# Kernel tuning notes

Hardware: AMD Instinct MI355X
Metric: run time of the kernel (lower is better)

## Reference

```python
import jax, jax.numpy as jnp
import numpy as np

TEMPERATURE = 0.07
B, D = 8192, 256

def _l2norm(x, axis=-1, eps=1e-12):
    # matches torch F.normalize(p=2): x / max(||x||, eps)
    n = jnp.sqrt(jnp.sum(x * x, axis=axis, keepdims=True))
    return x / jnp.maximum(n, eps)

def setup_inputs() -> dict:
    key = jax.random.key(0)
    k1, k2, k3 = jax.random.split(key, 3)
    return {
        "h_emb": jax.random.normal(k1, (B, D), dtype=jnp.float32),
        "r_emb": jax.random.normal(k2, (B, D), dtype=jnp.float32),
        "t_emb": jax.random.normal(k3, (B, D), dtype=jnp.float32),
    }

def reference(h_emb, r_emb, t_emb):
    # query = normalize(h + r); positives/negatives = normalize(t)
    q = _l2norm(h_emb + r_emb, axis=1)          # [B, D]
    t = _l2norm(t_emb, axis=1)                  # [B, D]
    # Dense in-batch similarity. The original builds logits = [pos, off-diag negs];
    # since the diagonal of sim IS the positive similarity, cross-entropy with
    # label 0 equals logsumexp over the full row minus the diagonal entry.
    sim = jnp.einsum('bd,nd->bn', q, t) / TEMPERATURE   # [B, B]
    pos = jnp.diagonal(sim)                              # [B]
    loss = jnp.mean(jax.nn.logsumexp(sim, axis=1) - pos)
    return loss
```

## Files before the change

### kernel.cpp

```cpp
#include <hip/hip_runtime.h>
#include <hip/hip_bf16.h>

#define B_DIM 8192
#define D_DIM 256
#define GRID_GEMM 512
#define NT 16

constexpr float INV_T = 14.285714285714286f;

typedef __bf16 bf16x8 __attribute__((ext_vector_type(8)));
typedef float  f32x4  __attribute__((ext_vector_type(4)));

#define GLOBAL_U32(p) ((const __attribute__((address_space(1))) unsigned int*)(p))
#define LDS_U32(p)    ((__attribute__((address_space(3))) unsigned int*)(p))

#define WAITCNT_VM0 0x0F70

__device__ inline unsigned short f2bf(float f) {
    union { float f; unsigned u; } x; x.f = f;
    unsigned r = x.u + 0x7fffu + ((x.u >> 16) & 1u);
    return (unsigned short)(r >> 16);
}

__global__ __launch_bounds__(256) void norm_kernel(
    const float* __restrict__ h, const float* __restrict__ r,
    const float* __restrict__ t,
    unsigned short* __restrict__ qws, unsigned short* __restrict__ tws,
    float* __restrict__ rowsum, float* __restrict__ diagsum, int* __restrict__ ticket)
{
    if (blockIdx.x == 0) {
        float4* rs4 = (float4*)rowsum;
#pragma unroll
        for (int i = 0; i < 8; ++i)
            rs4[threadIdx.x * 8 + i] = make_float4(0.f, 0.f, 0.f, 0.f);
        if (threadIdx.x == 0) { *diagsum = 0.f; *ticket = 0; }
    }

    const int wave = threadIdx.x >> 6;
    const int lane = threadIdx.x & 63;
    const int wg   = blockIdx.x * 4 + wave;

    const int kst  = lane >> 3;
    const int krun = (lane >> 1) & 3;
    const int sub8 = lane & 1;

#pragma unroll
    for (int i = 0; i < 2; ++i) {
        const int row = wg * 2 + i;
        {
            float4 a = ((const float4*)h)[row * 64 + lane];
            float4 b = ((const float4*)r)[row * 64 + lane];
            float4 v = make_float4(a.x + b.x, a.y + b.y, a.z + b.z, a.w + b.w);
            float s = v.x * v.x + v.y * v.y + v.z * v.z + v.w * v.w;
#pragma unroll
            for (int off = 32; off; off >>= 1) s += __shfl_xor(s, off, 64);
            float scale = INV_T / fmaxf(sqrtf(s), 1e-12f);
            ushort4 o;
            o.x = f2bf(v.x * scale); o.y = f2bf(v.y * scale);
            o.z = f2bf(v.z * scale); o.w = f2bf(v.w * scale);
            size_t slot16 = ((size_t)((row >> 4) * 8 + kst) * 64
                             + (size_t)(krun * 16 + (row & 15)));
            *(ushort4*)((unsigned char*)qws + slot16 * 16 + sub8 * 8) = o;
        }
        {
            float4 v = ((const float4*)t)[row * 64 + lane];
            float s = v.x * v.x + v.y * v.y + v.z * v.z + v.w * v.w;
#pragma unroll
            for (int off = 32; off; off >>= 1) s += __shfl_xor(s, off, 64);
            float scale = 1.0f / fmaxf(sqrtf(s), 1e-12f);
            ushort4 o;
            o.x = f2bf(v.x * scale); o.y = f2bf(v.y * scale);
            o.z = f2bf(v.z * scale); o.w = f2bf(v.w * scale);
            size_t slot16 = ((size_t)((row >> 4) * 8 + kst) * 64
                             + (size_t)(krun * 16 + (row & 15)));
            *(ushort4*)((unsigned char*)tws + slot16 * 16 + sub8 * 8) = o;
        }
    }
}

__global__ __launch_bounds__(256, 2) void gemm_lse_kernel(
    const unsigned char* __restrict__ qws, const unsigned char* __restrict__ tws,
    float* __restrict__ rowsum, float* __restrict__ diagsum,
    int* __restrict__ ticket, float* __restrict__ out)
{
    __shared__ __align__(16) unsigned char ldsB[4][32 * 512];
    __shared__ float wred[4];
    __shared__ int lastflag;

    const int tid  = threadIdx.x;
    const int lane = tid & 63;
    const int w    = tid >> 6;
    const int l15  = lane & 15;
    const int hi4  = lane >> 4;

    const int cc   = blockIdx.x & 15;
    const int rb   = blockIdx.x >> 4;
    const int row0 = rb * 256 + w * 64;
    const int col0 = cc * 512;
    const int tile0 = cc * 16;

#define STAGE(st, bufi)                                                      \
    {                                                                        \
        const unsigned char* gs = tws + (size_t)(tile0 + (st)) * 16384;      \
        _Pragma("unroll")                                                    \
        for (int it = 0; it < 4; ++it)                                       \
            __builtin_amdgcn_global_load_lds(                                \
                GLOBAL_U32(gs + (it * 256 + tid) * 16),                      \
                LDS_U32(&ldsB[bufi][(it * 256 + tid) * 16]), 16, 0, 0);      \
    }

    STAGE(0, 0);
    STAGE(1, 1);

    bf16x8 a[4][8];
    {
        const unsigned char* abase = qws + (size_t)row0 * 512 + lane * 16;
#pragma unroll
        for (int r = 0; r < 4; ++r)
#pragma unroll
            for (int kst = 0; kst < 8; ++kst)
                a[r][kst] = *(const bf16x8*)(abase + r * 8192 + kst * 1024);
    }

    float rowacc[16] = {};
    float diagacc = 0.f;

#define PROCESS_TILE(t)                                                      \
    {                                                                        \
        const unsigned char* bbuf = ldsB[(t) & 3] + lane * 16;               \
        f32x4 acc[4][2] = {};                                                \
        _Pragma("unroll")                                                    \
        for (int kst = 0; kst < 8; ++kst) {                                  \
            bf16x8 b0 = *(const bf16x8*)(bbuf + kst * 1024);                 \
            bf16x8 b1 = *(const bf16x8*)(bbuf + 8192 + kst * 1024);          \
            _Pragma("unroll")                                                \
            for (int r = 0; r < 4; ++r) {                                    \
                acc[r][0] = __builtin_amdgcn_mfma_f32_16x16x32_bf16(         \
                                a[r][kst], b0, acc[r][0], 0, 0, 0);          \
                acc[r][1] = __builtin_amdgcn_mfma_f32_16x16x32_bf16(         \
                                a[r][kst], b1, acc[r][1], 0, 0, 0);          \
            }                                                                \
        }                                                                    \
        _Pragma("unroll")                                                    \
        for (int r = 0; r < 4; ++r)                                          \
            _Pragma("unroll")                                                \
            for (int g = 0; g < 4; ++g)                                      \
                rowacc[r * 4 + g] += __expf(acc[r][0][g] - INV_T)            \
                                   + __expf(acc[r][1][g] - INV_T);           \
        const int c0t = col0 + (t) * 32;                                     \
        if (c0t == row0) {                                                   \
            _Pragma("unroll")                                                \
            for (int g = 0; g < 4; ++g)                                      \
                if (l15 == hi4 * 4 + g)                                      \
                    diagacc += acc[0][0][g] + acc[1][1][g];                  \
        }                                                                    \
        if (c0t == row0 + 32) {                                              \
            _Pragma("unroll")                                                \
            for (int g = 0; g < 4; ++g)                                      \
                if (l15 == hi4 * 4 + g)                                      \
                    diagacc += acc[2][0][g] + acc[3][1][g];                  \
        }                                                                    \
    }

    for (int r = 0; r < 8; ++r) {
        __builtin_amdgcn_s_waitcnt(WAITCNT_VM0);
        __builtin_amdgcn_s_barrier();
        if (r < 7) {
            STAGE(2 * r + 2, (2 * r + 2) & 3);
            STAGE(2 * r + 3, (2 * r + 3) & 3);
        }
        PROCESS_TILE(2 * r);
        PROCESS_TILE(2 * r + 1);
    }

#pragma unroll
    for (int rr = 0; rr < 16; ++rr) {
        float s = rowacc[rr];
        s += __shfl_xor(s, 1, 64);
        s += __shfl_xor(s, 2, 64);
        s += __shfl_xor(s, 4, 64);
        s += __shfl_xor(s, 8, 64);
        if (l15 == 0) {
            int grow = row0 + (rr >> 2) * 16 + hi4 * 4 + (rr & 3);
            atomicAdd(&rowsum[grow], s);
        }
    }

    float dsum = diagacc;
#pragma unroll
    for (int off = 32; off; off >>= 1) dsum += __shfl_xor(dsum, off, 64);
    if (lane == 0 && dsum != 0.f) atomicAdd(diagsum, dsum);

    __syncthreads();
    if (tid == 0) {
        __threadfence();
        int old = __hip_atomic_fetch_add(ticket, 1, __ATOMIC_ACQ_REL,
                                         __HIP_MEMORY_SCOPE_AGENT);
        lastflag = (old == GRID_GEMM - 1);
    }
    __syncthreads();
    if (!lastflag) return;

    float lsum = 0.f;
    for (int rr = tid; rr < B_DIM; rr += 256) {
        float rs = __hip_atomic_load(&rowsum[rr], __ATOMIC_RELAXED,
                                     __HIP_MEMORY_SCOPE_AGENT);
        lsum += __logf(rs);
    }
#pragma unroll
    for (int off = 32; off; off >>= 1) lsum += __shfl_xor(lsum, off, 64);
    if (lane == 0) wred[w] = lsum;
    __syncthreads();
    if (tid == 0) {
        float ds = __hip_atomic_load(diagsum, __ATOMIC_RELAXED,
                                     __HIP_MEMORY_SCOPE_AGENT);
        float total = wred[0] + wred[1] + wred[2] + wred[3]
                    + (float)B_DIM * INV_T
                    - ds;
        out[0] = total / (float)B_DIM;
    }
}

extern "C" void kernel_launch(void* const* d_in, const int* in_sizes, int n_in,
                              void* d_out, int out_size, void* d_ws, size_t ws_size,
                              hipStream_t stream)
{
    const float* h = (const float*)d_in[0];
    const float* r = (const float*)d_in[1];
    const float* t = (const float*)d_in[2];

    unsigned char* ws = (unsigned char*)d_ws;
    unsigned short* qws = (unsigned short*)ws;
    unsigned short* tws = (unsigned short*)(ws + 4u * 1024 * 1024);
    float* rowsum  = (float*)(ws + 8u * 1024 * 1024);
    float* diagsum = (float*)(ws + 8u * 1024 * 1024 + 32u * 1024);
    int*   ticket  = (int*)  (ws + 8u * 1024 * 1024 + 32u * 1024 + 16);

    norm_kernel<<<1024, 256, 0, stream>>>(h, r, t, qws, tws, rowsum, diagsum, ticket);
    gemm_lse_kernel<<<GRID_GEMM, 256, 0, stream>>>(
        (const unsigned char*)qws, (const unsigned char*)tws,
        rowsum, diagsum, ticket, (float*)d_out);
}
```

Baseline: 125.5 us.

## Give each wave private double-buffered B staging to remove block barriers

Replaces the block-wide shared 4-stage B buffer and per-round s_barrier with per-wave private double buffers. Each wave loads its own copy of every 16-column group via global_load_lds and waits with a partial vmcnt instead of synchronising the whole block. This removes barrier stalls between waves, but each wave now fetches the full B tile itself, so global/L2 traffic for B is four times higher. Correctness also relies on the wave-local ordering of the LDS DMA against ds reads.

Result: slower. 131.8 us (+5.0%).

```diff
diff --git a/kernel.cpp b/kernel.cpp
--- a/kernel.cpp
+++ b/kernel.cpp
@@ -5,6 +5,7 @@
 #define D_DIM 256
 #define GRID_GEMM 512
 #define NT 16
+#define NGRP 32
 
 constexpr float INV_T = 14.285714285714286f;
 
@@ -14,7 +15,7 @@
 #define GLOBAL_U32(p) ((const __attribute__((address_space(1))) unsigned int*)(p))
 #define LDS_U32(p)    ((__attribute__((address_space(3))) unsigned int*)(p))
 
-#define WAITCNT_VM0 0x0F70
+#define WAITCNT_VM8 0x0F78
 
 __device__ inline unsigned short f2bf(float f) {
     union { float f; unsigned u; } x; x.f = f;
@@ -83,7 +84,7 @@
     float* __restrict__ rowsum, float* __restrict__ diagsum,
     int* __restrict__ ticket, float* __restrict__ out)
 {
-    __shared__ __align__(16) unsigned char ldsB[4][32 * 512];
+    __shared__ __align__(16) unsigned char ldsB[4][2][8192];
     __shared__ float wred[4];
     __shared__ int lastflag;
 
@@ -97,20 +98,18 @@
     const int rb   = blockIdx.x >> 4;
     const int row0 = rb * 256 + w * 64;
     const int col0 = cc * 512;
-    const int tile0 = cc * 16;
-
-#define STAGE(st, bufi)                                                      \
+
+#define STAGE_W(g, bufi)                                                     \
     {                                                                        \
-        const unsigned char* gs = tws + (size_t)(tile0 + (st)) * 16384;      \
+        const unsigned char* gs = tws + ((size_t)cc * 32 + (g)) * 8192;      \
         _Pragma("unroll")                                                    \
-        for (int it = 0; it < 4; ++it)                                       \
+        for (int it = 0; it < 8; ++it)                                       \
             __builtin_amdgcn_global_load_lds(                                \
-                GLOBAL_U32(gs + (it * 256 + tid) * 16),                      \
-                LDS_U32(&ldsB[bufi][(it * 256 + tid) * 16]), 16, 0, 0);      \
-    }
-
-    STAGE(0, 0);
-    STAGE(1, 1);
+                GLOBAL_U32(gs + (it * 64 + lane) * 16),                      \
+                LDS_U32(&ldsB[w][bufi][(it * 64 + lane) * 16]), 16, 0, 0);   \
+    }
+
+    STAGE_W(0, 0);
 
     bf16x8 a[4][8];
     {
@@ -125,52 +124,47 @@
     float rowacc[16] = {};
     float diagacc = 0.f;
 
-#define PROCESS_TILE(t)                                                      \
-    {                                                                        \
-        const unsigned char* bbuf = ldsB[(t) & 3] + lane * 16;               \
-        f32x4 acc[4][2] = {};                                                \
-        _Pragma("unroll")                                                    \
-        for (int kst = 0; kst < 8; ++kst) {                                  \
-            bf16x8 b0 = *(const bf16x8*)(bbuf + kst * 1024);                 \
-            bf16x8 b1 = *(const bf16x8*)(bbuf + 8192 + kst * 1024);          \
-            _Pragma("unroll")                                                \
-            for (int r = 0; r < 4; ++r) {                                    \
-                acc[r][0] = __builtin_amdgcn_mfma_f32_16x16x32_bf16(         \
-                                a[r][kst], b0, acc[r][0], 0, 0, 0);          \
-                acc[r][1] = __builtin_amdgcn_mfma_f32_16x16x32_bf16(         \
-                                a[r][kst], b1, acc[r][1], 0, 0, 0);          \
-            }                                                                \
-        }                                                                    \
-        _Pragma("unroll")                                                    \
-        for (int r = 0; r < 4; ++r)                                          \
-            _Pragma("unroll")                                                \
-            for (int g = 0; g < 4; ++g)                                      \
-                rowacc[r * 4 + g] += __expf(acc[r][0][g] - INV_T)            \
-                                   + __expf(acc[r][1][g] - INV_T);           \
-        const int c0t = col0 + (t) * 32;                                     \
-        if (c0t == row0) {                                                   \
-            _Pragma("unroll")                                                \
-            for (int g = 0; g < 4; ++g)                                      \
-                if (l15 == hi4 * 4 + g)                                      \
-                    diagacc += acc[0][0][g] + acc[1][1][g];                  \
-        }                                                                    \
-        if (c0t == row0 + 32) {                                              \
-            _Pragma("unroll")                                                \
-            for (int g = 0; g < 4; ++g)                                      \
-                if (l15 == hi4 * 4 + g)                                      \
-                    diagacc += acc[2][0][g] + acc[3][1][g];                  \
-        }                                                                    \
-    }
-
-    for (int r = 0; r < 8; ++r) {
-        __builtin_amdgcn_s_waitcnt(WAITCNT_VM0);
-        __builtin_amdgcn_s_barrier();
-        if (r < 7) {
-            STAGE(2 * r + 2, (2 * r + 2) & 3);
-            STAGE(2 * r + 3, (2 * r + 3) & 3);
-        }
-        PROCESS_TILE(2 * r);
-        PROCESS_TILE(2 * r + 1);
+    for (int t = 0; t < NT; ++t) {
+        f32x4 acc[4][2] = {};
+#pragma unroll
+        for (int cg = 0; cg < 2; ++cg) {
+            const int g = t * 2 + cg;
+            const int gn = (g + 1 < NGRP) ? g + 1 : NGRP - 1;
+            STAGE_W(gn, (g + 1) & 1);
+            __builtin_amdgcn_s_waitcnt(WAITCNT_VM8);
+            __builtin_amdgcn_sched_barrier(0);
+
+            const unsigned char* bbuf = &ldsB[w][g & 1][0] + lane * 16;
+#pragma unroll
+            for (int kst = 0; kst < 8; ++kst) {
+                bf16x8 b = *(const bf16x8*)(bbuf + kst * 1024);
+#pragma unroll
+                for (int r = 0; r < 4; ++r)
+                    acc[r][cg] = __builtin_amdgcn_mfma_f32_16x16x32_bf16(
+                                     a[r][kst], b, acc[r][cg], 0, 0, 0);
+            }
+        }
+
+#pragma unroll
+        for (int r = 0; r < 4; ++r)
+#pragma unroll
+            for (int g2 = 0; g2 < 4; ++g2)
+                rowacc[r * 4 + g2] += __expf(acc[r][0][g2] - INV_T)
+                                    + __expf(acc[r][1][g2] - INV_T);
+
+        const int c0t = col0 + t * 32;
+        if (c0t == row0) {
+#pragma unroll
+            for (int g2 = 0; g2 < 4; ++g2)
+                if (l15 == hi4 * 4 + g2)
+                    diagacc += acc[0][0][g2] + acc[1][1][g2];
+        }
+        if (c0t == row0 + 32) {
+#pragma unroll
+            for (int g2 = 0; g2 < 4; ++g2)
+                if (l15 == hi4 * 4 + g2)
+                    diagacc += acc[2][0][g2] + acc[3][1][g2];
+        }
     }
 
 #pragma unroll
```

## Use 512-thread GEMM blocks with deeper 8-buffer LDS prefetch pipeline

Applied to the files above, without the earlier changes.

Doubles the GEMM block size to 512 threads (8 waves covering 512 rows) and halves the grid. The shared B tile staged in LDS is now reused by twice as many waves. The LDS ring grows to 8 buffers with three stages prefetched ahead, and the wait becomes a partial vmcnt so loads stay in flight across iterations. In the last iterations the loop re-stages the final tile pair into buffers that have already been consumed, which is redundant traffic. The larger LDS footprint and bigger blocks may reduce occupancy, and with 256 blocks the CUs may not all be filled.

Result: faster. 119.9 us (-4.4%).

```diff
diff --git a/kernel.cpp b/kernel.cpp
--- a/kernel.cpp
+++ b/kernel.cpp
@@ -3,7 +3,7 @@
 
 #define B_DIM 8192
 #define D_DIM 256
-#define GRID_GEMM 512
+#define GRID_GEMM 256
 #define NT 16
 
 constexpr float INV_T = 14.285714285714286f;
@@ -14,7 +14,7 @@
 #define GLOBAL_U32(p) ((const __attribute__((address_space(1))) unsigned int*)(p))
 #define LDS_U32(p)    ((__attribute__((address_space(3))) unsigned int*)(p))
 
-#define WAITCNT_VM0 0x0F70
+#define WAITCNT_VM8 0x0F78
 
 __device__ inline unsigned short f2bf(float f) {
     union { float f; unsigned u; } x; x.f = f;
@@ -72,19 +72,21 @@
             o.x = f2bf(v.x * scale); o.y = f2bf(v.y * scale);
             o.z = f2bf(v.z * scale); o.w = f2bf(v.w * scale);
             size_t slot16 = ((size_t)((row >> 4) * 8 + kst) * 64
-                             + (size_t)(krun * 16 + (row & 15)));
+                             + (size_t)(krun * 16 + (row & 31 & 15)));
+            slot16 = ((size_t)((row >> 4) * 8 + kst) * 64
+                      + (size_t)(krun * 16 + (row & 15)));
             *(ushort4*)((unsigned char*)tws + slot16 * 16 + sub8 * 8) = o;
         }
     }
 }
 
-__global__ __launch_bounds__(256, 2) void gemm_lse_kernel(
+__global__ __launch_bounds__(512, 2) void gemm_lse_kernel(
     const unsigned char* __restrict__ qws, const unsigned char* __restrict__ tws,
     float* __restrict__ rowsum, float* __restrict__ diagsum,
     int* __restrict__ ticket, float* __restrict__ out)
 {
-    __shared__ __align__(16) unsigned char ldsB[4][32 * 512];
-    __shared__ float wred[4];
+    __shared__ __align__(16) unsigned char ldsB[8][16384];
+    __shared__ float wred[8];
     __shared__ int lastflag;
 
     const int tid  = threadIdx.x;
@@ -95,7 +97,7 @@
 
     const int cc   = blockIdx.x & 15;
     const int rb   = blockIdx.x >> 4;
-    const int row0 = rb * 256 + w * 64;
+    const int row0 = rb * 512 + w * 64;
     const int col0 = cc * 512;
     const int tile0 = cc * 16;
 
@@ -103,14 +105,15 @@
     {                                                                        \
         const unsigned char* gs = tws + (size_t)(tile0 + (st)) * 16384;      \
         _Pragma("unroll")                                                    \
-        for (int it = 0; it < 4; ++it)                                       \
+        for (int it = 0; it < 2; ++it)                                       \
             __builtin_amdgcn_global_load_lds(                                \
-                GLOBAL_U32(gs + (it * 256 + tid) * 16),                      \
-                LDS_U32(&ldsB[bufi][(it * 256 + tid) * 16]), 16, 0, 0);      \
-    }
-
-    STAGE(0, 0);
-    STAGE(1, 1);
+                GLOBAL_U32(gs + (it * 512 + tid) * 16),                      \
+                LDS_U32(&ldsB[bufi][(it * 512 + tid) * 16]), 16, 0, 0);      \
+    }
+
+    STAGE(0, 0); STAGE(1, 1);
+    STAGE(2, 2); STAGE(3, 3);
+    STAGE(4, 4); STAGE(5, 5);
 
     bf16x8 a[4][8];
     {
@@ -127,12 +130,12 @@
 
 #define PROCESS_TILE(t)                                                      \
     {                                                                        \
-        const unsigned char* bbuf = ldsB[(t) & 3] + lane * 16;               \
+        const unsigned char* bbuf = ldsB[(t) & 7] + lane * 16;               \
         f32x4 acc[4][2] = {};                                                \
         _Pragma("unroll")                                                    \
         for (int kst = 0; kst < 8; ++kst) {                                  \
             bf16x8 b0 = *(const bf16x8*)(bbuf + kst * 1024);                 \
-            bf16x8 b1 = *(const bf16x8*)(bbuf + 8192 + kst * 1024);          \
+            bf16x8 b1 = *(const bf16x8*)(bbuf + 8192 + kst * 1024);         \
             _Pragma("unroll")                                                \
             for (int r = 0; r < 4; ++r) {                                    \
                 acc[r][0] = __builtin_amdgcn_mfma_f32_16x16x32_bf16(         \
@@ -144,31 +147,30 @@
         _Pragma("unroll")                                                    \
         for (int r = 0; r < 4; ++r)                                          \
             _Pragma("unroll")                                                \
-            for (int g = 0; g < 4; ++g)                                      \
-                rowacc[r * 4 + g] += __expf(acc[r][0][g] - INV_T)            \
-                                   + __expf(acc[r][1][g] - INV_T);           \
+            for (int g2 = 0; g2 < 4; ++g2)                                   \
+                rowacc[r * 4 + g2] += __expf(acc[r][0][g2] - INV_T)          \
+                                    + __expf(acc[r][1][g2] - INV_T);         \
         const int c0t = col0 + (t) * 32;                                     \
         if (c0t == row0) {                                                   \
             _Pragma("unroll")                                                \
-            for (int g = 0; g < 4; ++g)                                      \
-                if (l15 == hi4 * 4 + g)                                      \
-                    diagacc += acc[0][0][g] + acc[1][1][g];                  \
+            for (int g2 = 0; g2 < 4; ++g2)                                   \
+                if (l15 == hi4 * 4 + g2)                                     \
+                    diagacc += acc[0][0][g2] + acc[1][1][g2];                \
         }                                                                    \
         if (c0t == row0 + 32) {                                              \
             _Pragma("unroll")                                                \
-            for (int g = 0; g < 4; ++g)                                      \
-                if (l15 == hi4 * 4 + g)                                      \
-                    diagacc += acc[2][0][g] + acc[3][1][g];                  \
+            for (int g2 = 0; g2 < 4; ++g2)                                   \
+                if (l15 == hi4 * 4 + g2)                                     \
+                    diagacc += acc[2][0][g2] + acc[3][1][g2];                \
         }                                                                    \
     }
 
     for (int r = 0; r < 8; ++r) {
-        __builtin_amdgcn_s_waitcnt(WAITCNT_VM0);
+        __builtin_amdgcn_s_waitcnt(WAITCNT_VM8);
         __builtin_amdgcn_s_barrier();
-        if (r < 7) {
-            STAGE(2 * r + 2, (2 * r + 2) & 3);
-            STAGE(2 * r + 3, (2 * r + 3) & 3);
-        }
+        const int p = (r + 3 < 8) ? r + 3 : 7;
+        STAGE(2 * p,     (2 * r + 6) & 7);
+        STAGE(2 * p + 1, (2 * r + 7) & 7);
         PROCESS_TILE(2 * r);
         PROCESS_TILE(2 * r + 1);
     }
@@ -202,7 +204,7 @@
     if (!lastflag) return;
 
     float lsum = 0.f;
-    for (int rr = tid; rr < B_DIM; rr += 256) {
+    for (int rr = tid; rr < B_DIM; rr += 512) {
         float rs = __hip_atomic_load(&rowsum[rr], __ATOMIC_RELAXED,
                                      __HIP_MEMORY_SCOPE_AGENT);
         lsum += __logf(rs);
@@ -212,11 +214,11 @@
     if (lane == 0) wred[w] = lsum;
     __syncthreads();
     if (tid == 0) {
-        float ds = __hip_atomic_load(diagsum, __ATOMIC_RELAXED,
-                                     __HIP_MEMORY_SCOPE_AGENT);
         float total = wred[0] + wred[1] + wred[2] + wred[3]
+                    + wred[4] + wred[5] + wred[6] + wred[7]
                     + (float)B_DIM * INV_T
-                    - ds;
+                    - __hip_atomic_load(diagsum, __ATOMIC_RELAXED,
+                                        __HIP_MEMORY_SCOPE_AGENT);
         out[0] = total / (float)B_DIM;
     }
 }
@@ -237,7 +239,7 @@
     int*   ticket  = (int*)  (ws + 8u * 1024 * 1024 + 32u * 1024 + 16);
 
     norm_kernel<<<1024, 256, 0, stream>>>(h, r, t, qws, tws, rowsum, diagsum, ticket);
-    gemm_lse_kernel<<<GRID_GEMM, 256, 0, stream>>>(
+    gemm_lse_kernel<<<GRID_GEMM, 512, 0, stream>>>(
         (const unsigned char*)qws, (const unsigned char*)tws,
         rowsum, diagsum, ticket, (float*)d_out);
 }
```
